# Kernel tuning notes

Measured on AMD Instinct MI355X. Metric: run time of the kernel, lower is better.

## Reference

```python
import jax, jax.numpy as jnp
import numpy as np

T = 10          # time_steps
IN_DIM = 784    # 28*28
HID = 256
NCLS = 47
THRESH = 1.0
TAU_MEM = 2.0   # LIF membrane time constant
TAU_OUT = 2.0   # readout EMA time constant


@jax.custom_vjp
def spike_fn(u):
    # Heaviside spike on (v - threshold), surrogate gradient in bwd.
    return (u >= 0.0).astype(u.dtype)

def _spike_fwd(u):
    return spike_fn(u), u

def _spike_bwd(u, g):
    # sigmoid surrogate derivative, slope 4
    s = jax.nn.sigmoid(4.0 * u)
    return (g * 4.0 * s * (1.0 - s),)

spike_fn.defvjp(_spike_fwd, _spike_bwd)


def setup_inputs() -> dict:
    key = jax.random.key(0)
    k1, k2, k3 = jax.random.split(key, 3)
    x = jax.random.uniform(k1, (4096, 1, 28, 28), dtype=jnp.float32)
    W1 = jax.random.normal(k2, (IN_DIM, HID), dtype=jnp.float32) / np.float32(np.sqrt(IN_DIM))
    b1 = jnp.zeros((HID,), jnp.float32)
    Wr = jax.random.normal(k3, (HID, NCLS), dtype=jnp.float32) / np.float32(np.sqrt(HID))
    br = jnp.zeros((NCLS,), jnp.float32)
    return {"x": x, "W1": W1, "b1": b1, "Wr": Wr, "br": br}


def reference(x, W1, b1, Wr, br):
    B = x.shape[0]
    xf = x.reshape(B, -1)  # [B, 784] pixel intensities in [0,1]
    # rate_encode_flat: Bernoulli(p=pixel) spikes per timestep -> [T, B, 784]
    ek = jax.random.key(42)
    seq = (jax.random.uniform(ek, (T, B, IN_DIM), dtype=xf.dtype) < xf[None]).astype(xf.dtype)

    def step(carry, s_t):
        v_hid, v_out = carry
        I_hid = s_t @ W1 + b1                      # [B, HID]
        v_hid = v_hid + (I_hid - v_hid) / TAU_MEM  # leaky integration
        spk = spike_fn(v_hid - THRESH)             # spike emission
        v_hid = v_hid * (1.0 - spk)                # hard reset to 0
        I = spk @ Wr + br                          # [B, NCLS]
        v_out = v_out + (I - v_out) / TAU_OUT      # output EMA
        return (v_hid, v_out), None

    init = (jnp.zeros((B, HID), xf.dtype), jnp.zeros((B, NCLS), xf.dtype))
    (_, v_out), _ = jax.lax.scan(step, init, seq)
    return v_out
```

## Files before the change

kernel.cpp:

```cpp
#include <hip/hip_runtime.h>
#include <stdint.h>


#define T_STEPS 10
#define BATCH   4096
#define IN_DIM  784
#define HID     256
#define NCLS    47
#define NROWS   (T_STEPS * BATCH)
#define KWORDS  25
#define KPAD    800
#define M_TILE  160

#define WS_IALL_OFF 0u
#define WS_W1HI_OFF 46039040u
#define WS_W1MD_OFF (46039040u + 409600u)
#define WS_W1LO_OFF (46039040u + 819200u)

typedef __attribute__((ext_vector_type(8))) short    bf16x8;
typedef __attribute__((ext_vector_type(4))) float    f32x4;
typedef __attribute__((ext_vector_type(4))) uint32_t u32x4;

__device__ __forceinline__ uint32_t rotl32(uint32_t x, uint32_t r) {
    return __builtin_amdgcn_alignbit(x, x, 32u - r);
}

__device__ __forceinline__ uint32_t tf_hash(uint32_t lo) {
    const uint32_t ks1 = 42u;
    const uint32_t ks2 = 0x1BD11BDAu ^ 42u;
    uint32_t x0 = 0u;
    uint32_t x1 = lo + ks1;
#define TF_RND(r) { x0 += x1; x1 = rotl32(x1, r); x1 ^= x0; }
    TF_RND(13) TF_RND(15) TF_RND(26) TF_RND(6)
    x0 += ks1; x1 += ks2 + 1u;
    TF_RND(17) TF_RND(29) TF_RND(16) TF_RND(24)
    x0 += ks2; x1 += 2u;
    TF_RND(13) TF_RND(15) TF_RND(26) TF_RND(6)
    x1 += ks1 + 3u;
    TF_RND(17) TF_RND(29) TF_RND(16) TF_RND(24)
    x0 += ks1; x1 += ks2 + 4u;
    TF_RND(13) TF_RND(15) TF_RND(26) TF_RND(6)
    x0 += ks2; x1 += 5u;
#undef TF_RND
    return x0 ^ x1;
}

__device__ __forceinline__ uint32_t hash2(uint32_t ib, const float* xp) {
    float2 xx = *(const float2*)xp;
    uint32_t w = 0u;
    w |= ((float)(tf_hash(ib + 0u) >> 9) < xx.x * 8388608.0f) ? 0x3F80u : 0u;
    w |= ((float)(tf_hash(ib + 1u) >> 9) < xx.y * 8388608.0f) ? 0x3F800000u : 0u;
    return w;
}

__global__ __launch_bounds__(256) void splitk_k(
        const float* __restrict__ W1, ushort* __restrict__ hiT,
        ushort* __restrict__ midT, ushort* __restrict__ loT) {
    int n = blockIdx.x;
    for (int k = threadIdx.x; k < KPAD; k += 256) {
        float w = (k < IN_DIM) ? W1[k * HID + n] : 0.0f;
        uint32_t u = __float_as_uint(w);
        uint32_t hb = (u + 0x7FFFu + ((u >> 16) & 1u)) >> 16;
        float hf = __uint_as_float(hb << 16);
        float r1 = w - hf;
        uint32_t u1 = __float_as_uint(r1);
        uint32_t mb = (u1 + 0x7FFFu + ((u1 >> 16) & 1u)) >> 16;
        float mf2 = __uint_as_float(mb << 16);
        float r2 = r1 - mf2;
        uint32_t u2 = __float_as_uint(r2);
        uint32_t lb = (u2 + 0x7FFFu + ((u2 >> 16) & 1u)) >> 16;
        hiT [n * KPAD + k] = (ushort)hb;
        midT[n * KPAD + k] = (ushort)mb;
        loT [n * KPAD + k] = (ushort)lb;
    }
}

#define LDS_B0  20480
#define B_BUFSZ 49152
#define A_BUFSZ 10240

__global__ __launch_bounds__(512, 2) void fused_gemm_k(
        const ushort* __restrict__ hiT, const ushort* __restrict__ midT,
        const ushort* __restrict__ loT, const float* __restrict__ b1,
        const float* __restrict__ x, float* __restrict__ I_all) {
    __shared__ __align__(16) char lds[118784];

    const int tid = threadIdx.x;
    const int l   = tid & 63;
    const int wv  = tid >> 6;
    const int wm  = wv >> 2;
    const int wn  = wv & 3;
    const int m0  = blockIdx.x * M_TILE;

    f32x4 acc[5][4] = {};

    const int q   = l >> 4;
    const int sig = q ^ (l & 3) ^ ((l >> 2) & 3);
    const int a_rd = wm * 5120 + ((l & 15) << 6) + (sig << 4);
    const int b_rd = (((wn << 6) + (l & 15)) << 6) + (sig << 4);

    const ushort* hi_p[2];
    const ushort* md_p[2];
    const ushort* lo_p[2];
    int bdst[2];
#pragma unroll
    for (int i = 0; i < 2; ++i) {
        int s  = (i << 9) + tid;
        int n  = s >> 2;
        int qs = s & 3;
        int qd = qs ^ (n & 3) ^ ((n >> 2) & 3);
        size_t eoff = (size_t)n * KPAD + ((size_t)qd << 3);
        hi_p[i] = hiT  + eoff;
        md_p[i] = midT + eoff;
        lo_p[i] = loT  + eoff;
        bdst[i] = ((i << 9) + (wv << 6)) << 4;
    }

    int      adst[5];
    const float* txp[5];
    uint32_t tib[5];
    int      tpp[5];
#pragma unroll
    for (int s = 0; s < 5; ++s) {
        int tau = tid + (s << 9);
        int row = tau >> 4;
        int p   = tau & 15;
        int qd  = (p >> 2) ^ (row & 3) ^ ((row >> 2) & 3);
        adst[s] = (row << 6) + (qd << 4) + ((p & 3) << 2);
        int rowg = m0 + row;
        txp[s]  = x + (size_t)(rowg & (BATCH - 1)) * IN_DIM + (p << 1);
        tib[s]  = (uint32_t)rowg * (uint32_t)IN_DIM + (uint32_t)(p << 1);
        tpp[s]  = p;
    }

#define STAGE_B(koff, bbase) \
    _Pragma("unroll") \
    for (int i = 0; i < 2; ++i) { \
        __builtin_amdgcn_global_load_lds( \
            (const __attribute__((address_space(1))) void*)(hi_p[i] + (koff)), \
            (__attribute__((address_space(3))) void*)(lds + (bbase) + bdst[i]), \
            16, 0, 0); \
        __builtin_amdgcn_global_load_lds( \
            (const __attribute__((address_space(1))) void*)(md_p[i] + (koff)), \
            (__attribute__((address_space(3))) void*)(lds + (bbase) + 16384 + bdst[i]), \
            16, 0, 0); \
        __builtin_amdgcn_global_load_lds( \
            (const __attribute__((address_space(1))) void*)(lo_p[i] + (koff)), \
            (__attribute__((address_space(3))) void*)(lds + (bbase) + 32768 + bdst[i]), \
            16, 0, 0); \
    }

#define HASH_SLAB(koff, abase, is_tail) \
    _Pragma("unroll") \
    for (int s = 0; s < 5; ++s) { \
        uint32_t w_ = 0u; \
        if (!(is_tail) || tpp[s] < 8) \
            w_ = hash2(tib[s] + (uint32_t)(koff), txp[s] + (koff)); \
        *(uint32_t*)(lds + (abase) + adst[s]) = w_; \
    }

    STAGE_B(0, LDS_B0)
    HASH_SLAB(0, 0, false)
    __syncthreads();

    int cur = 0;
#pragma unroll 1
    for (int kw = 0; kw < KWORDS; ++kw) {
        const int nxt = cur ^ 1;

        if (kw < KWORDS - 1) {
            const int koff = (kw + 1) << 5;
            STAGE_B(koff, LDS_B0 + nxt * B_BUFSZ)
        }

        const char* A = lds + cur * A_BUFSZ;
        const char* B = lds + LDS_B0 + cur * B_BUFSZ;
        bf16x8 af[5];
        bf16x8 bfr[3][4];
#pragma unroll
        for (int mt = 0; mt < 5; ++mt)
            af[mt] = *(const bf16x8*)(A + a_rd + (mt << 10));
#pragma unroll
        for (int nt = 0; nt < 4; ++nt) {
            bfr[0][nt] = *(const bf16x8*)(B + b_rd + (nt << 10));
            bfr[1][nt] = *(const bf16x8*)(B + 16384 + b_rd + (nt << 10));
            bfr[2][nt] = *(const bf16x8*)(B + 32768 + b_rd + (nt << 10));
        }

        if (kw < KWORDS - 1) {
            const int koff = (kw + 1) << 5;
            const bool tail = (kw + 1 == KWORDS - 1);
            HASH_SLAB(koff, nxt * A_BUFSZ, tail)
        }

#pragma unroll
        for (int nt = 0; nt < 4; ++nt) {
#pragma unroll
            for (int mt = 0; mt < 5; ++mt) {
                acc[mt][nt] = __builtin_amdgcn_mfma_f32_16x16x32_bf16(af[mt], bfr[0][nt], acc[mt][nt], 0, 0, 0);
                acc[mt][nt] = __builtin_amdgcn_mfma_f32_16x16x32_bf16(af[mt], bfr[1][nt], acc[mt][nt], 0, 0, 0);
                acc[mt][nt] = __builtin_amdgcn_mfma_f32_16x16x32_bf16(af[mt], bfr[2][nt], acc[mt][nt], 0, 0, 0);
            }
        }

        __syncthreads();
        cur = nxt;
    }
#undef STAGE_B
#undef HASH_SLAB

    const int c0 = l & 15;
    float b1v[4];
#pragma unroll
    for (int nt = 0; nt < 4; ++nt)
        b1v[nt] = b1[(wn << 6) + (nt << 4) + c0];
#pragma unroll
    for (int mt = 0; mt < 5; ++mt) {
#pragma unroll
        for (int nt = 0; nt < 4; ++nt) {
            int col = (wn << 6) + (nt << 4) + c0;
#pragma unroll
            for (int r = 0; r < 4; ++r) {
                int row = m0 + wm * 80 + (mt << 4) + (q << 2) + r;
                I_all[(size_t)row * HID + col] = acc[mt][nt][r] + b1v[nt];
            }
        }
    }
}

__global__ __launch_bounds__(256) void scanout_k(
        const float* __restrict__ I_all, const float* __restrict__ Wr,
        const float* __restrict__ br, float* __restrict__ out) {
    __shared__ float gl[4 * 256];
    const int tid = threadIdx.x;
    const int b0  = blockIdx.x << 2;

#pragma unroll
    for (int b = 0; b < 4; ++b) {
        const float* p = I_all + ((size_t)(b0 + b) << 8) + tid;
        float v = 0.f, ga = 0.f, wt = 0.0009765625f;
#pragma unroll
        for (int t = 0; t < T_STEPS; ++t) {
            float I = p[(size_t)t * BATCH * HID];
            v = v + (I - v) * 0.5f;
            if (v >= 1.0f) { ga += wt; v = 0.f; }
            wt += wt;
        }
        gl[(b << 8) + tid] = ga;
    }
    __syncthreads();

    const int wv = tid >> 6;
    const int c  = tid & 63;
    if (c >= NCLS) return;
    const float* gb = &gl[wv << 8];
    float acc = 0.f;
    for (int h4 = 0; h4 < 64; ++h4) {
        float w0 = Wr[((h4 << 2) + 0) * NCLS + c];
        float w1 = Wr[((h4 << 2) + 1) * NCLS + c];
        float w2 = Wr[((h4 << 2) + 2) * NCLS + c];
        float w3 = Wr[((h4 << 2) + 3) * NCLS + c];
        float4 gg = *(const float4*)&gb[h4 << 2];
        acc = fmaf(gg.x, w0, acc);
        acc = fmaf(gg.y, w1, acc);
        acc = fmaf(gg.z, w2, acc);
        acc = fmaf(gg.w, w3, acc);
    }
    float brv = br[c] * 0.9990234375f;
    out[(b0 + wv) * NCLS + c] = acc + brv;
}

extern "C" void kernel_launch(void* const* d_in, const int* in_sizes, int n_in,
                              void* d_out, int out_size, void* d_ws, size_t ws_size,
                              hipStream_t stream) {
    const float* x  = (const float*)d_in[0];
    const float* W1 = (const float*)d_in[1];
    const float* b1 = (const float*)d_in[2];
    const float* Wr = (const float*)d_in[3];
    const float* br = (const float*)d_in[4];
    float* out = (float*)d_out;

    float*  I_all = (float*) ((char*)d_ws + WS_IALL_OFF);
    ushort* w1hi  = (ushort*)((char*)d_ws + WS_W1HI_OFF);
    ushort* w1md  = (ushort*)((char*)d_ws + WS_W1MD_OFF);
    ushort* w1lo  = (ushort*)((char*)d_ws + WS_W1LO_OFF);

    splitk_k<<<HID, 256, 0, stream>>>(W1, w1hi, w1md, w1lo);
    fused_gemm_k<<<NROWS / M_TILE, 512, 0, stream>>>(w1hi, w1md, w1lo, b1, x, I_all);
    scanout_k<<<BATCH / 4, 256, 0, stream>>>(I_all, Wr, br, out);
}
```

Before: 185.0 us.

## Interleave hash-encoding tasks with MFMA chunks and peel last K iteration

Splits the per-iteration Bernoulli hash generation into five tasks and interleaves each with a chunk of 12 MFMAs, so integer ALU work can overlap matrix-core work instead of running as a separate phase. The final K iteration is peeled out to drop the per-iteration branches. Launch bounds change from 2 to 1 blocks per SM, which gives the compiler more registers. The LDS footprint (~116KB) likely already limited residency, so this should cost little occupancy, but the extra registers may change scheduling.

```diff
diff --git a/kernel.cpp b/kernel.cpp
--- a/kernel.cpp
+++ b/kernel.cpp
@@ -79,7 +79,7 @@
 #define B_BUFSZ 49152
 #define A_BUFSZ 10240
 
-__global__ __launch_bounds__(512, 2) void fused_gemm_k(
+__global__ __launch_bounds__(512, 1) void fused_gemm_k(
         const ushort* __restrict__ hiT, const ushort* __restrict__ midT,
         const ushort* __restrict__ loT, const float* __restrict__ b1,
         const float* __restrict__ x, float* __restrict__ I_all) {
@@ -150,64 +150,73 @@
             16, 0, 0); \
     }
 
-#define HASH_SLAB(koff, abase, is_tail) \
+#define HASH_TASK(s, koff, abase, is_tail) { \
+    uint32_t w_ = 0u; \
+    if (!(is_tail) || tpp[s] < 8) \
+        w_ = hash2(tib[s] + (uint32_t)(koff), txp[s] + (koff)); \
+    *(uint32_t*)(lds + (abase) + adst[s]) = w_; }
+
+#define MFMA_CHUNK(s) \
     _Pragma("unroll") \
-    for (int s = 0; s < 5; ++s) { \
-        uint32_t w_ = 0u; \
-        if (!(is_tail) || tpp[s] < 8) \
-            w_ = hash2(tib[s] + (uint32_t)(koff), txp[s] + (koff)); \
-        *(uint32_t*)(lds + (abase) + adst[s]) = w_; \
+    for (int m = (s) * 12; m < (s) * 12 + 12; ++m) { \
+        const int nt_ = m / 15, r_ = m % 15, pl_ = r_ / 5, mt_ = r_ % 5; \
+        acc[mt_][nt_] = __builtin_amdgcn_mfma_f32_16x16x32_bf16( \
+            af[mt_], bfr[pl_][nt_], acc[mt_][nt_], 0, 0, 0); \
+    }
+
+#define PRELOAD_FRAGS(bufidx) \
+    const char* A = lds + (bufidx) * A_BUFSZ; \
+    const char* B = lds + LDS_B0 + (bufidx) * B_BUFSZ; \
+    bf16x8 af[5]; \
+    bf16x8 bfr[3][4]; \
+    _Pragma("unroll") \
+    for (int mt = 0; mt < 5; ++mt) \
+        af[mt] = *(const bf16x8*)(A + a_rd + (mt << 10)); \
+    _Pragma("unroll") \
+    for (int nt = 0; nt < 4; ++nt) { \
+        bfr[0][nt] = *(const bf16x8*)(B + b_rd + (nt << 10)); \
+        bfr[1][nt] = *(const bf16x8*)(B + 16384 + b_rd + (nt << 10)); \
+        bfr[2][nt] = *(const bf16x8*)(B + 32768 + b_rd + (nt << 10)); \
     }
 
     STAGE_B(0, LDS_B0)
-    HASH_SLAB(0, 0, false)
+    HASH_TASK(0, 0, 0, false)
+    HASH_TASK(1, 0, 0, false)
+    HASH_TASK(2, 0, 0, false)
+    HASH_TASK(3, 0, 0, false)
+    HASH_TASK(4, 0, 0, false)
     __syncthreads();
 
     int cur = 0;
 #pragma unroll 1
-    for (int kw = 0; kw < KWORDS; ++kw) {
-        const int nxt = cur ^ 1;
-
-        if (kw < KWORDS - 1) {
-            const int koff = (kw + 1) << 5;
-            STAGE_B(koff, LDS_B0 + nxt * B_BUFSZ)
-        }
-
-        const char* A = lds + cur * A_BUFSZ;
-        const char* B = lds + LDS_B0 + cur * B_BUFSZ;
-        bf16x8 af[5];
-        bf16x8 bfr[3][4];
-#pragma unroll
-        for (int mt = 0; mt < 5; ++mt)
-            af[mt] = *(const bf16x8*)(A + a_rd + (mt << 10));
-#pragma unroll
-        for (int nt = 0; nt < 4; ++nt) {
-            bfr[0][nt] = *(const bf16x8*)(B + b_rd + (nt << 10));
-            bfr[1][nt] = *(const bf16x8*)(B + 16384 + b_rd + (nt << 10));
-            bfr[2][nt] = *(const bf16x8*)(B + 32768 + b_rd + (nt << 10));
-        }
-
-        if (kw < KWORDS - 1) {
-            const int koff = (kw + 1) << 5;
-            const bool tail = (kw + 1 == KWORDS - 1);
-            HASH_SLAB(koff, nxt * A_BUFSZ, tail)
-        }
-
-#pragma unroll
-        for (int nt = 0; nt < 4; ++nt) {
-#pragma unroll
-            for (int mt = 0; mt < 5; ++mt) {
-                acc[mt][nt] = __builtin_amdgcn_mfma_f32_16x16x32_bf16(af[mt], bfr[0][nt], acc[mt][nt], 0, 0, 0);
-                acc[mt][nt] = __builtin_amdgcn_mfma_f32_16x16x32_bf16(af[mt], bfr[1][nt], acc[mt][nt], 0, 0, 0);
-                acc[mt][nt] = __builtin_amdgcn_mfma_f32_16x16x32_bf16(af[mt], bfr[2][nt], acc[mt][nt], 0, 0, 0);
-            }
-        }
+    for (int kw = 0; kw < KWORDS - 1; ++kw) {
+        const int  nxt  = cur ^ 1;
+        const int  koff = (kw + 1) << 5;
+        const bool tail = (kw == KWORDS - 2);
+
+        STAGE_B(koff, LDS_B0 + nxt * B_BUFSZ)
+
+        PRELOAD_FRAGS(cur)
+
+        const int ab = nxt * A_BUFSZ;
+        HASH_TASK(0, koff, ab, tail)  MFMA_CHUNK(0)
+        HASH_TASK(1, koff, ab, tail)  MFMA_CHUNK(1)
+        HASH_TASK(2, koff, ab, tail)  MFMA_CHUNK(2)
+        HASH_TASK(3, koff, ab, tail)  MFMA_CHUNK(3)
+        HASH_TASK(4, koff, ab, tail)  MFMA_CHUNK(4)
 
         __syncthreads();
         cur = nxt;
     }
+
+    {
+        PRELOAD_FRAGS(cur)
+        MFMA_CHUNK(0) MFMA_CHUNK(1) MFMA_CHUNK(2) MFMA_CHUNK(3) MFMA_CHUNK(4)
+    }
 #undef STAGE_B
-#undef HASH_SLAB
+#undef HASH_TASK
+#undef MFMA_CHUNK
+#undef PRELOAD_FRAGS
 
     const int c0 = l & 15;
     float b1v[4];
```

Measured after the change: 186.8 us. About the same (+0.9%).
